# Performance work log

Measured on AMD Instinct MI355X. Metric: run time of the kernel, lower is better.

## Reference

```python
import jax, jax.numpy as jnp
import numpy as np

V, E, H, S, B, MAX_OOV = 50000, 256, 512, 500, 64, 50


def setup_inputs() -> dict:
    key = jax.random.key(0)
    ks = jax.random.split(key, 22)
    s = 0.02  # param init scale
    return {
        "input_token": jax.random.randint(ks[0], (B, 1), 0, V),
        "encoder_hidden_states": jax.random.normal(ks[1], (S, B, 2 * H), jnp.float32),
        "projected_encoder_hidden_states": jax.random.normal(ks[2], (S, B, H), jnp.float32),
        "src_mask": jnp.ones((B, S), dtype=bool),
        "prev_hidden": jax.random.normal(ks[3], (1, B, H), jnp.float32),
        "encoder_batch_extended_vocab": jax.random.randint(ks[4], (B, S), 0, V + MAX_OOV),
        "batch_max_oov": MAX_OOV,
        # learned parameters
        "emb": jax.random.normal(ks[5], (V, E), jnp.float32) * s,
        "attn_Wq": jax.random.normal(ks[6], (H, H), jnp.float32) * s,   # query_layer, no bias
        "attn_We": jax.random.normal(ks[7], (1, H), jnp.float32) * s,   # energy_layer, no bias
        "gru_Wih": jax.random.normal(ks[8], (3 * H, E + 2 * H), jnp.float32) * s,
        "gru_Whh": jax.random.normal(ks[9], (3 * H, H), jnp.float32) * s,
        "gru_bih": jax.random.normal(ks[10], (3 * H,), jnp.float32) * s,
        "gru_bhh": jax.random.normal(ks[11], (3 * H,), jnp.float32) * s,
        "lin_W": jax.random.normal(ks[12], (H, E + 3 * H), jnp.float32) * s,
        "lin_b": jax.random.normal(ks[13], (H,), jnp.float32) * s,
        "pg_W": jax.random.normal(ks[14], (1, E + 3 * H), jnp.float32) * s,
        "pg_b": jax.random.normal(ks[15], (1,), jnp.float32) * s,
        "out_W": jax.random.normal(ks[16], (V, H), jnp.float32) * s,
        "out_b": jax.random.normal(ks[17], (V,), jnp.float32) * s,
    }


def _forward(input_token, enc_h, proj_key, prev_hidden, ext_vocab, max_oov,
             emb, attn_Wq, attn_We, gru_Wih, gru_Whh, gru_bih, gru_bhh,
             lin_W, lin_b, pg_W, pg_b, out_W, out_b):
    b = input_token.shape[0]
    embed = jnp.transpose(emb[input_token], (1, 0, 2))  # [1,B,E]

    # Bahdanau attention (softmax over source dim 0; mask unused, as in source)
    q = jnp.einsum('tbh,oh->tbo', prev_hidden, attn_Wq)            # [1,B,H]
    scores = jnp.einsum('sbh,oh->sb', jnp.tanh(q + proj_key), attn_We)  # [S,B]
    alphas = jax.nn.softmax(scores, axis=0)                        # [S,B]
    context = jnp.einsum('sb,sbd->bd', alphas, enc_h)[None]        # [1,B,2H]
    attention_dist = alphas.T                                      # [B,S]

    # GRU cell (torch gate order: r, z, n)
    x = jnp.concatenate([embed, context], axis=2)[0]               # [B,E+2H]
    h = prev_hidden[0]                                             # [B,H]
    gi = x @ gru_Wih.T + gru_bih                                   # [B,3H]
    gh = h @ gru_Whh.T + gru_bhh
    i_r, i_z, i_n = jnp.split(gi, 3, axis=1)
    h_r, h_z, h_n = jnp.split(gh, 3, axis=1)
    r = jax.nn.sigmoid(i_r + h_r)
    z = jax.nn.sigmoid(i_z + h_z)
    n = jnp.tanh(i_n + r * h_n)
    h_new = (1.0 - z) * n + z * h                                  # [B,H]
    rnn_output = h_new[None]                                       # [1,B,H]

    concat = jnp.concatenate([embed, rnn_output, context], axis=2)  # [1,B,E+3H]
    p_gen = jax.nn.sigmoid(jnp.einsum('tbf,of->tbo', concat, pg_W) + pg_b)  # [1,B,1]
    lin = jnp.einsum('tbf,of->tbo', concat, lin_W) + lin_b          # [1,B,H]
    logits = jnp.einsum('tbh,vh->tbv', lin, out_W) + out_b          # [1,B,V]

    gen_prob = p_gen * jax.nn.softmax(logits, axis=2)               # [1,B,V]
    attn_prob = ((1.0 - p_gen) * attention_dist[None])[0]           # [B,S]

    ext = jnp.concatenate(
        [gen_prob, jnp.zeros((1, b, max_oov), gen_prob.dtype)], axis=2) + 1e-12  # [1,B,V+oov]
    rows = jnp.arange(b)[:, None]
    merged = ext.at[0, rows, ext_vocab].add(attn_prob)              # scatter_add over vocab dim
    output = jnp.log(merged)
    return output, h_new[None]


def reference(input_token, encoder_hidden_states, projected_encoder_hidden_states,
              src_mask, prev_hidden, encoder_batch_extended_vocab, batch_max_oov,
              emb, attn_Wq, attn_We, gru_Wih, gru_Whh, gru_bih, gru_bhh,
              lin_W, lin_b, pg_W, pg_b, out_W, out_b):
    return _forward(input_token, encoder_hidden_states, projected_encoder_hidden_states,
                    prev_hidden, encoder_batch_extended_vocab, batch_max_oov,
                    emb, attn_Wq, attn_We, gru_Wih, gru_Whh, gru_bih, gru_bhh,
                    lin_W, lin_b, pg_W, pg_b, out_W, out_b)
```

## Files before the change

### kernel.cpp

```cpp
#include <hip/hip_runtime.h>
#include <hip/hip_bf16.h>
#include <math.h>

namespace {
constexpr int V = 50000, E = 256, H = 512, S = 500, B = 64, OOVN = 50;
constexpr int VEXT = V + OOVN;
constexpr int CCAT = E + 3 * H;
constexpr int G3 = 3 * H;
constexpr int NLB = 391;

typedef __attribute__((ext_vector_type(8))) short short8;
typedef __attribute__((ext_vector_type(4))) float f32x4;

__device__ __forceinline__ float wsum(float v) {
#pragma unroll
  for (int off = 32; off > 0; off >>= 1) v += __shfl_xor(v, off, 64);
  return v;
}
__device__ __forceinline__ float sigmoidf(float x) { return 1.f / (1.f + __expf(-x)); }
__device__ __forceinline__ float fast_tanh(float x) {
  x = fminf(fmaxf(x, -15.f), 15.f);
  float e = __expf(2.f * x);
  return __fdividef(e - 1.f, e + 1.f);
}
__device__ __forceinline__ void smerge_s(float& m, float& l, float om, float ol) {
  float nm = fmaxf(m, om);
  if (nm == -INFINITY) { m = nm; return; }
  l = l * __expf(m - nm) + ol * __expf(om - nm);
  m = nm;
}

__device__ __forceinline__ short bf16_rn_s(float f) {
  __hip_bfloat16 h = __float2bfloat16(f);
  return __builtin_bit_cast(short, h);
}
__device__ __forceinline__ void hilo1(float f, short* hi, short* lo) {
  unsigned u = __float_as_uint(f);
  *hi = (short)(u >> 16);
  *lo = bf16_rn_s(f - __uint_as_float(u & 0xffff0000u));
}
__device__ __forceinline__ void hilo8(float4 a, float4 b, short8& hi, short8& lo) {
  float f[8] = {a.x, a.y, a.z, a.w, b.x, b.y, b.z, b.w};
#pragma unroll
  for (int i = 0; i < 8; ++i) {
    unsigned u = __float_as_uint(f[i]);
    hi[i] = (short)(u >> 16);
    lo[i] = bf16_rn_s(f[i] - __uint_as_float(u & 0xffff0000u));
  }
}

template <int KSTEPS>
__device__ __forceinline__ void gemm16(const short* __restrict__ Xhi,
                                       const short* __restrict__ Xlo, int ldx, int xk0,
                                       const float* __restrict__ W, int ldw, int wk0,
                                       int n0, float* __restrict__ C, int ldc) {
  const int l = threadIdx.x & 63;
  const int r16 = l & 15, q16 = l >> 4;
  f32x4 acc[4];
#pragma unroll
  for (int t = 0; t < 4; ++t) acc[t] = (f32x4){0.f, 0.f, 0.f, 0.f};

  const float* wp = W + (size_t)(n0 + r16) * ldw + wk0 + q16 * 8;
  const short* xh[4];
  const short* xl[4];
#pragma unroll
  for (int t = 0; t < 4; ++t) {
    int row = t * 16 + r16;
    xh[t] = Xhi + (size_t)row * ldx + xk0 + q16 * 8;
    xl[t] = Xlo + (size_t)row * ldx + xk0 + q16 * 8;
  }

#pragma unroll
  for (int ks = 0; ks < KSTEPS; ++ks) {
    const int ko = ks * 32;
    float4 w0 = *reinterpret_cast<const float4*>(wp + ko);
    float4 w1 = *reinterpret_cast<const float4*>(wp + ko + 4);
    short8 whi, wlo;
    hilo8(w0, w1, whi, wlo);
#pragma unroll
    for (int t = 0; t < 4; ++t) {
      short8 ah = *reinterpret_cast<const short8*>(xh[t] + ko);
      short8 al = *reinterpret_cast<const short8*>(xl[t] + ko);
      acc[t] = __builtin_amdgcn_mfma_f32_16x16x32_bf16(ah, whi, acc[t], 0, 0, 0);
      acc[t] = __builtin_amdgcn_mfma_f32_16x16x32_bf16(al, whi, acc[t], 0, 0, 0);
      acc[t] = __builtin_amdgcn_mfma_f32_16x16x32_bf16(ah, wlo, acc[t], 0, 0, 0);
    }
  }
#pragma unroll
  for (int t = 0; t < 4; ++t) {
#pragma unroll
    for (int r = 0; r < 4; ++r) {
      int row = t * 16 + q16 * 4 + r;
      C[(size_t)row * ldc + n0 + r16] = acc[t][r];
    }
  }
}

__global__ void k_prep(const int* __restrict__ tok, const float* __restrict__ emb,
                       const float* __restrict__ prevh, float* __restrict__ cc,
                       short* __restrict__ cch, short* __restrict__ ccl,
                       short* __restrict__ hh, short* __restrict__ hl) {
  int i = blockIdx.x * 256 + threadIdx.x;
  hilo1(prevh[i], &hh[i], &hl[i]);
  if (i < 16384) {
    int b = i >> 8, e = i & 255;
    float v = emb[(size_t)tok[b] * E + e];
    cc[b * CCAT + e] = v;
    hilo1(v, &cch[b * CCAT + e], &ccl[b * CCAT + e]);
  }
}

__global__ void __launch_bounds__(256) k_gemm_qgh(
    const short* __restrict__ hh, const short* __restrict__ hl,
    const float* __restrict__ Wq, const float* __restrict__ Whh,
    float* __restrict__ qpart, float* __restrict__ ghp) {
  int w = blockIdx.x * 4 + (threadIdx.x >> 6);
  if (w < 128) {
    int c = w >> 5, nt = w & 31;
    gemm16<4>(hh, hl, H, c * 128, Wq, H, c * 128, nt * 16,
              qpart + (size_t)c * 64 * H, H);
  } else {
    int w2 = w - 128;
    int c = w2 / 96, nt = w2 % 96;
    gemm16<8>(hh, hl, H, c * 256, Whh, H, c * 256, nt * 16,
              ghp + (size_t)c * 64 * G3, G3);
  }
}

__global__ void k_scores(const float* __restrict__ qpart, const float* __restrict__ pk,
                         const float* __restrict__ We, float* __restrict__ scores) {
  int lane = threadIdx.x & 63;
  int gw = blockIdx.x * 4 + (threadIdx.x >> 6);
  int s = gw >> 6, b = gw & 63;
  const float* q0 = qpart + b * H + lane * 8;
  const float* kr = pk + ((size_t)s * B + b) * H + lane * 8;
  const float* er = We + lane * 8;
  float part = 0.f;
#pragma unroll
  for (int i = 0; i < 2; ++i) {
    float4 qa = *reinterpret_cast<const float4*>(q0 + i * 4);
    float4 qb = *reinterpret_cast<const float4*>(q0 + 64 * H + i * 4);
    float4 qc = *reinterpret_cast<const float4*>(q0 + 128 * H + i * 4);
    float4 qd = *reinterpret_cast<const float4*>(q0 + 192 * H + i * 4);
    float4 kv = *reinterpret_cast<const float4*>(kr + i * 4);
    float4 ev = *reinterpret_cast<const float4*>(er + i * 4);
    part += fast_tanh(qa.x + qb.x + qc.x + qd.x + kv.x) * ev.x +
            fast_tanh(qa.y + qb.y + qc.y + qd.y + kv.y) * ev.y +
            fast_tanh(qa.z + qb.z + qc.z + qd.z + kv.z) * ev.z +
            fast_tanh(qa.w + qb.w + qc.w + qd.w + kv.w) * ev.w;
  }
  part = wsum(part);
  if (lane == 0) scores[s * B + b] = part;
}

__global__ void k_softmax_s(const float* __restrict__ scores, float* __restrict__ alphasT) {
  int b = blockIdx.x, t = threadIdx.x;
  int w = t >> 6, lane = t & 63;
  __shared__ float rm[8], rl[8];
  float v = (t < S) ? scores[t * B + b] : -INFINITY;
  float m = v;
#pragma unroll
  for (int off = 32; off > 0; off >>= 1) m = fmaxf(m, __shfl_xor(m, off, 64));
  if (lane == 0) rm[w] = m;
  __syncthreads();
  float bm = rm[0];
#pragma unroll
  for (int i = 1; i < 8; ++i) bm = fmaxf(bm, rm[i]);
  float e = (t < S) ? __expf(v - bm) : 0.f;
  float sw = wsum(e);
  if (lane == 0) rl[w] = sw;
  __syncthreads();
  float tot = rl[0];
#pragma unroll
  for (int i = 1; i < 8; ++i) tot += rl[i];
  if (t < S) alphasT[b * S + t] = e / tot;
}

__global__ void k_ctx(const float* __restrict__ alphasT, const float* __restrict__ ench,
                      float* __restrict__ ctxp) {
  int b = blockIdx.x, chf = blockIdx.y, sh = blockIdx.z;
  int t = threadIdx.x;
  __shared__ float sa[250];
  if (t < 250) sa[t] = alphasT[b * S + sh * 250 + t];
  __syncthreads();
  const float* base = ench + ((size_t)(sh * 250) * B + b) * 1024 + chf * 512 + t;
  float a0 = 0.f, a1 = 0.f;
#pragma unroll 8
  for (int s = 0; s < 250; s += 2) {
    a0 += sa[s] * base[(size_t)s * (B * 1024)];
    a1 += sa[s + 1] * base[(size_t)(s + 1) * (B * 1024)];
  }
  ctxp[((sh * B + b) * 1024) + chf * 512 + t] = a0 + a1;
}

__global__ void k_ctx2(const float* __restrict__ ctxp, float* __restrict__ cc,
                       short* __restrict__ cch, short* __restrict__ ccl) {
  int b = blockIdx.x, t = threadIdx.x;
  int c = t * 4;
  float4 v0 = *reinterpret_cast<const float4*>(&ctxp[(b * 1024) + c]);
  float4 v1 = *reinterpret_cast<const float4*>(&ctxp[((B + b) * 1024) + c]);
  float r[4] = {v0.x + v1.x, v0.y + v1.y, v0.z + v1.z, v0.w + v1.w};
#pragma unroll
  for (int i = 0; i < 4; ++i) {
    int col = 768 + c + i;
    cc[b * CCAT + col] = r[i];
    hilo1(r[i], &cch[b * CCAT + col], &ccl[b * CCAT + col]);
  }
}

__global__ void __launch_bounds__(256) k_gemm_big(
    const short* __restrict__ cch, const short* __restrict__ ccl,
    const float* __restrict__ Wih, const float* __restrict__ linW,
    float* __restrict__ gip, float* __restrict__ linpart) {
  int w = blockIdx.x * 4 + (threadIdx.x >> 6);
  if (w < 480) {
    int c = w / 96, nt = w % 96;
    int xk0 = (c == 0) ? 0 : 768 + (c - 1) * 256;
    int wk0 = c * 256;
    gemm16<8>(cch, ccl, CCAT, xk0, Wih, 1280, wk0, nt * 16,
              gip + (size_t)c * 64 * G3, G3);
  } else {
    int w2 = w - 480;
    int c = w2 >> 5, nt = w2 & 31;
    int k0 = (c == 0) ? 0 : 768 + (c - 1) * 256;
    gemm16<8>(cch, ccl, CCAT, k0, linW, CCAT, k0, nt * 16,
              linpart + (size_t)c * 64 * H, H);
  }
}

__global__ void k_gates(const float* __restrict__ gip, const float* __restrict__ ghp,
                        const float* __restrict__ bih, const float* __restrict__ bhh,
                        const float* __restrict__ prevh, const float* __restrict__ pgW,
                        const float* __restrict__ pgb, float* __restrict__ cc,
                        short* __restrict__ cch, short* __restrict__ ccl,
                        float* __restrict__ hout, float* __restrict__ pgsum) {
  int b = blockIdx.x, j = threadIdx.x;
  float ir = bih[j], iz = bih[512 + j], in_ = bih[1024 + j];
#pragma unroll
  for (int c = 0; c < 5; ++c) {
    const float* g = gip + (size_t)c * 64 * G3 + b * G3;
    ir += g[j]; iz += g[512 + j]; in_ += g[1024 + j];
  }
  float hr = bhh[j], hz = bhh[512 + j], hn = bhh[1024 + j];
#pragma unroll
  for (int c = 0; c < 2; ++c) {
    const float* g = ghp + (size_t)c * 64 * G3 + b * G3;
    hr += g[j]; hz += g[512 + j]; hn += g[1024 + j];
  }
  float r = sigmoidf(ir + hr);
  float z = sigmoidf(iz + hz);
  float n = fast_tanh(in_ + r * hn);
  float h = prevh[b * H + j];
  float hnew = (1.f - z) * n + z * h;
  hout[b * H + j] = hnew;
  cc[b * CCAT + E + j] = hnew;
  hilo1(hnew, &cch[b * CCAT + E + j], &ccl[b * CCAT + E + j]);
  float acc = hnew * pgW[E + j];
  acc += cc[b * CCAT + 768 + j] * pgW[768 + j];
  acc += cc[b * CCAT + 1280 + j] * pgW[1280 + j];
  if (j < 256) acc += cc[b * CCAT + j] * pgW[j];
  acc = wsum(acc);
  __shared__ float sl[8];
  int w = j >> 6, lane = j & 63;
  if (lane == 0) sl[w] = acc;
  __syncthreads();
  if (j == 0) {
    float tot = pgb[0];
#pragma unroll
    for (int i = 0; i < 8; ++i) tot += sl[i];
    pgsum[b] = tot;
  }
}

__global__ void __launch_bounds__(256) k_gemm_linh(const short* __restrict__ cch,
                                                   const short* __restrict__ ccl,
                                                   const float* __restrict__ linW,
                                                   float* __restrict__ linpart) {
  int w = blockIdx.x * 4 + (threadIdx.x >> 6);
  int c = w >> 5, nt = w & 31;
  int k0 = 256 + c * 256;
  gemm16<8>(cch, ccl, CCAT, k0, linW, CCAT, k0, nt * 16,
            linpart + (size_t)(5 + c) * 64 * H, H);
}

__global__ void k_linfin(const float* __restrict__ linpart, const float* __restrict__ linb,
                         short* __restrict__ lh) {
  int idx = blockIdx.x * 256 + threadIdx.x;
  int b = idx >> 9, o = idx & 511;
  float v = linb[o];
#pragma unroll
  for (int c = 0; c < 7; ++c) v += linpart[(size_t)c * 64 * H + b * H + o];
  lh[idx] = bf16_rn_s(v);
}

__global__ void __launch_bounds__(512) k_gemm_logits(
    const short* __restrict__ lh, const float* __restrict__ outW,
    const float* __restrict__ outb, float* __restrict__ logits,
    float* __restrict__ pm, float* __restrict__ pl) {
  __shared__ __align__(16) short xs[64 * 512];
  __shared__ float pml[8][64][2];
  char* xb = reinterpret_cast<char*>(xs);
  int tid = threadIdx.x;
#pragma unroll
  for (int k = 0; k < 8; ++k) {
    int m = k * 512 + tid;
    int row = m >> 6;
    short8 v = *reinterpret_cast<const short8*>(lh + (size_t)m * 8);
    int byte = (m * 16) ^ ((row & 7) << 4);
    *reinterpret_cast<short8*>(xb + byte) = v;
  }
  __syncthreads();
  const int l = tid & 63;
  const int r16 = l & 15, q16 = l >> 4;
  const int wid = tid >> 6;
  const int waveId = blockIdx.x * 8 + wid;
  const bool active = waveId < V / 16;
  if (active) {
    const int n0 = waveId * 16;
    f32x4 acc[4];
#pragma unroll
    for (int t = 0; t < 4; ++t) acc[t] = (f32x4){0.f, 0.f, 0.f, 0.f};
    const float* wp = outW + (size_t)(n0 + r16) * H + q16 * 8;
    int arow[4], aswz[4];
#pragma unroll
    for (int t = 0; t < 4; ++t) {
      int row = t * 16 + r16;
      arow[t] = row * 1024 + q16 * 16;
      aswz[t] = (row & 7) << 4;
    }
#pragma unroll
    for (int ks = 0; ks < 16; ++ks) {
      float4 w0 = *reinterpret_cast<const float4*>(wp + ks * 32);
      float4 w1 = *reinterpret_cast<const float4*>(wp + ks * 32 + 4);
      short8 wh;
      wh[0] = bf16_rn_s(w0.x); wh[1] = bf16_rn_s(w0.y);
      wh[2] = bf16_rn_s(w0.z); wh[3] = bf16_rn_s(w0.w);
      wh[4] = bf16_rn_s(w1.x); wh[5] = bf16_rn_s(w1.y);
      wh[6] = bf16_rn_s(w1.z); wh[7] = bf16_rn_s(w1.w);
#pragma unroll
      for (int t = 0; t < 4; ++t) {
        short8 a = *reinterpret_cast<const short8*>(xb + ((arow[t] + ks * 64) ^ aswz[t]));
        acc[t] = __builtin_amdgcn_mfma_f32_16x16x32_bf16(a, wh, acc[t], 0, 0, 0);
      }
    }
    float bv = outb[n0 + r16];
#pragma unroll
    for (int t = 0; t < 4; ++t) {
#pragma unroll
      for (int r = 0; r < 4; ++r) {
        float y = acc[t][r] + bv;
        int row = t * 16 + q16 * 4 + r;
        logits[(size_t)row * V + n0 + r16] = y;
        float m = y;
#pragma unroll
        for (int off = 8; off > 0; off >>= 1) m = fmaxf(m, __shfl_xor(m, off, 64));
        float e = __expf(y - m);
#pragma unroll
        for (int off = 8; off > 0; off >>= 1) e += __shfl_xor(e, off, 64);
        if (r16 == 0) { pml[wid][row][0] = m; pml[wid][row][1] = e; }
      }
    }
  } else if (r16 == 0) {
#pragma unroll
    for (int t = 0; t < 4; ++t)
#pragma unroll
      for (int r = 0; r < 4; ++r) {
        int row = t * 16 + q16 * 4 + r;
        pml[wid][row][0] = -INFINITY;
        pml[wid][row][1] = 0.f;
      }
  }
  __syncthreads();
  if (tid < 64) {
    float m = pml[0][tid][0], lv = pml[0][tid][1];
#pragma unroll
    for (int i = 1; i < 8; ++i) smerge_s(m, lv, pml[i][tid][0], pml[i][tid][1]);
    pm[blockIdx.x * 64 + tid] = m;
    pl[blockIdx.x * 64 + tid] = lv;
  }
}

__global__ void k_final(const float* __restrict__ logits, const float* __restrict__ pm,
                        const float* __restrict__ pl, const float* __restrict__ pgsum,
                        const int* __restrict__ extv, const float* __restrict__ alphasT,
                        float* __restrict__ out) {
  int b = blockIdx.x, c = blockIdx.y, t = threadIdx.x;
  __shared__ float sp_[5056];
  __shared__ float rm[4], rl[4];
  float m = -INFINITY, lv = 0.f;
  for (int i = t; i < NLB; i += 256) smerge_s(m, lv, pm[i * 64 + b], pl[i * 64 + b]);
#pragma unroll
  for (int off = 32; off > 0; off >>= 1) {
    float om = __shfl_xor(m, off, 64), ol = __shfl_xor(lv, off, 64);
    smerge_s(m, lv, om, ol);
  }
  int w = t >> 6, lane = t & 63;
  if (lane == 0) { rm[w] = m; rl[w] = lv; }
  __syncthreads();
  m = rm[0]; lv = rl[0];
#pragma unroll
  for (int i = 1; i < 4; ++i) smerge_s(m, lv, rm[i], rl[i]);
  float pg = sigmoidf(pgsum[b]);
  float scale = pg / lv;
  const int base = c * 5000;
  const int len = (c == 9) ? 5050 : 5000;
  const float* lr = logits + (size_t)b * V + base;
  for (int i = t; i < len; i += 256)
    sp_[i] = (i < 5000) ? scale * __expf(lr[i] - m) + 1e-12f : 1e-12f;
  __syncthreads();
  float wgt = 1.f - pg;
  for (int s = t; s < S; s += 256) {
    int idx = extv[b * S + s] - base;
    if ((unsigned)idx < (unsigned)len) atomicAdd(&sp_[idx], wgt * alphasT[b * S + s]);
  }
  __syncthreads();
  float* orow = out + (size_t)b * VEXT + base;
  for (int i = t; i < len; i += 256) orow[i] = logf(sp_[i]);
}
}

extern "C" void kernel_launch(void* const* d_in, const int* in_sizes, int n_in,
                              void* d_out, int out_size, void* d_ws, size_t ws_size,
                              hipStream_t stream) {
  const int*   tok   = (const int*)d_in[0];
  const float* ench  = (const float*)d_in[1];
  const float* pk    = (const float*)d_in[2];
  const float* prevh = (const float*)d_in[4];
  const int*   extv  = (const int*)d_in[5];
  const float* emb   = (const float*)d_in[7];
  const float* Wq    = (const float*)d_in[8];
  const float* We    = (const float*)d_in[9];
  const float* Wih   = (const float*)d_in[10];
  const float* Whh   = (const float*)d_in[11];
  const float* bih   = (const float*)d_in[12];
  const float* bhh   = (const float*)d_in[13];
  const float* linW  = (const float*)d_in[14];
  const float* linb  = (const float*)d_in[15];
  const float* pgW   = (const float*)d_in[16];
  const float* pgb   = (const float*)d_in[17];
  const float* outW  = (const float*)d_in[18];
  const float* outb  = (const float*)d_in[19];

  float* out = (float*)d_out;
  float* ws = (float*)d_ws;

  float* qpart   = ws;
  float* scores  = qpart + 131072;
  float* alphasT = scores + 32000;
  float* ctxp    = alphasT + 32000;
  float* cc      = ctxp + 131072;
  float* gip     = cc + 114688;
  float* ghp     = gip + 491520;
  float* linpart = ghp + 196608;
  float* pgsum   = linpart + 229376;
  float* logits  = pgsum + 64;
  float* pm      = logits + 3200000;
  float* pl      = pm + 25024;
  short* sp      = (short*)(pl + 25024);
  short* cch = sp;
  short* ccl = cch + 114688;
  short* hh  = ccl + 114688;
  short* hl  = hh + 32768;
  short* lh  = hl + 32768;
  float* hout = out + (size_t)B * VEXT;

  k_prep<<<dim3(128), dim3(256), 0, stream>>>(tok, emb, prevh, cc, cch, ccl, hh, hl);
  k_gemm_qgh<<<dim3(80), dim3(256), 0, stream>>>(hh, hl, Wq, Whh, qpart, ghp);
  k_scores<<<dim3(8000), dim3(256), 0, stream>>>(qpart, pk, We, scores);
  k_softmax_s<<<dim3(B), dim3(512), 0, stream>>>(scores, alphasT);
  k_ctx<<<dim3(64, 2, 2), dim3(512), 0, stream>>>(alphasT, ench, ctxp);
  k_ctx2<<<dim3(B), dim3(256), 0, stream>>>(ctxp, cc, cch, ccl);
  k_gemm_big<<<dim3(160), dim3(256), 0, stream>>>(cch, ccl, Wih, linW, gip, linpart);
  k_gates<<<dim3(B), dim3(512), 0, stream>>>(gip, ghp, bih, bhh, prevh, pgW, pgb, cc, cch,
                                             ccl, hout, pgsum);
  k_gemm_linh<<<dim3(16), dim3(256), 0, stream>>>(cch, ccl, linW, linpart);
  k_linfin<<<dim3(128), dim3(256), 0, stream>>>(linpart, linb, lh);
  k_gemm_logits<<<dim3(NLB), dim3(512), 0, stream>>>(lh, outW, outb, logits, pm, pl);
  k_final<<<dim3(B, 10), dim3(256), 0, stream>>>(logits, pm, pl, pgsum, extv, alphasT, out);
}
```

Before: 162.8 us.

## Fuse prep and small kernels, split activations to bf16 inside GEMMs

```diff
diff --git a/kernel.cpp b/kernel.cpp
--- a/kernel.cpp
+++ b/kernel.cpp
@@ -29,15 +29,9 @@
   l = l * __expf(m - nm) + ol * __expf(om - nm);
   m = nm;
 }
-
 __device__ __forceinline__ short bf16_rn_s(float f) {
   __hip_bfloat16 h = __float2bfloat16(f);
   return __builtin_bit_cast(short, h);
-}
-__device__ __forceinline__ void hilo1(float f, short* hi, short* lo) {
-  unsigned u = __float_as_uint(f);
-  *hi = (short)(u >> 16);
-  *lo = bf16_rn_s(f - __uint_as_float(u & 0xffff0000u));
 }
 __device__ __forceinline__ void hilo8(float4 a, float4 b, short8& hi, short8& lo) {
   float f[8] = {a.x, a.y, a.z, a.w, b.x, b.y, b.z, b.w};
@@ -50,26 +44,17 @@
 }
 
 template <int KSTEPS>
-__device__ __forceinline__ void gemm16(const short* __restrict__ Xhi,
-                                       const short* __restrict__ Xlo, int ldx, int xk0,
-                                       const float* __restrict__ W, int ldw, int wk0,
-                                       int n0, float* __restrict__ C, int ldc) {
+__device__ __forceinline__ void gemm_core_f32(const float* __restrict__ X, int ldx,
+                                              int xk0, const float* __restrict__ W,
+                                              int ldw, int wk0, int n0, f32x4 acc[4]) {
   const int l = threadIdx.x & 63;
   const int r16 = l & 15, q16 = l >> 4;
-  f32x4 acc[4];
 #pragma unroll
   for (int t = 0; t < 4; ++t) acc[t] = (f32x4){0.f, 0.f, 0.f, 0.f};
-
   const float* wp = W + (size_t)(n0 + r16) * ldw + wk0 + q16 * 8;
-  const short* xh[4];
-  const short* xl[4];
-#pragma unroll
-  for (int t = 0; t < 4; ++t) {
-    int row = t * 16 + r16;
-    xh[t] = Xhi + (size_t)row * ldx + xk0 + q16 * 8;
-    xl[t] = Xlo + (size_t)row * ldx + xk0 + q16 * 8;
-  }
-
+  const float* xp[4];
+#pragma unroll
+  for (int t = 0; t < 4; ++t) xp[t] = X + (size_t)(t * 16 + r16) * ldx + xk0 + q16 * 8;
 #pragma unroll
   for (int ks = 0; ks < KSTEPS; ++ks) {
     const int ko = ks * 32;
@@ -79,56 +64,66 @@
     hilo8(w0, w1, whi, wlo);
 #pragma unroll
     for (int t = 0; t < 4; ++t) {
-      short8 ah = *reinterpret_cast<const short8*>(xh[t] + ko);
-      short8 al = *reinterpret_cast<const short8*>(xl[t] + ko);
+      float4 x0 = *reinterpret_cast<const float4*>(xp[t] + ko);
+      float4 x1 = *reinterpret_cast<const float4*>(xp[t] + ko + 4);
+      short8 ah, al;
+      hilo8(x0, x1, ah, al);
       acc[t] = __builtin_amdgcn_mfma_f32_16x16x32_bf16(ah, whi, acc[t], 0, 0, 0);
       acc[t] = __builtin_amdgcn_mfma_f32_16x16x32_bf16(al, whi, acc[t], 0, 0, 0);
       acc[t] = __builtin_amdgcn_mfma_f32_16x16x32_bf16(ah, wlo, acc[t], 0, 0, 0);
     }
   }
-#pragma unroll
-  for (int t = 0; t < 4; ++t) {
+}
+template <int KSTEPS>
+__device__ __forceinline__ void gemm_store_f32(const float* X, int ldx, int xk0,
+                                               const float* W, int ldw, int wk0, int n0,
+                                               float* C, int ldc) {
+  f32x4 acc[4];
+  gemm_core_f32<KSTEPS>(X, ldx, xk0, W, ldw, wk0, n0, acc);
+  const int l = threadIdx.x & 63;
+  const int r16 = l & 15, q16 = l >> 4;
+#pragma unroll
+  for (int t = 0; t < 4; ++t)
 #pragma unroll
     for (int r = 0; r < 4; ++r) {
       int row = t * 16 + q16 * 4 + r;
       C[(size_t)row * ldc + n0 + r16] = acc[t][r];
     }
-  }
-}
-
-__global__ void k_prep(const int* __restrict__ tok, const float* __restrict__ emb,
-                       const float* __restrict__ prevh, float* __restrict__ cc,
-                       short* __restrict__ cch, short* __restrict__ ccl,
-                       short* __restrict__ hh, short* __restrict__ hl) {
-  int i = blockIdx.x * 256 + threadIdx.x;
-  hilo1(prevh[i], &hh[i], &hl[i]);
-  if (i < 16384) {
-    int b = i >> 8, e = i & 255;
-    float v = emb[(size_t)tok[b] * E + e];
-    cc[b * CCAT + e] = v;
-    hilo1(v, &cch[b * CCAT + e], &ccl[b * CCAT + e]);
-  }
-}
-
-__global__ void __launch_bounds__(256) k_gemm_qgh(
-    const short* __restrict__ hh, const short* __restrict__ hl,
-    const float* __restrict__ Wq, const float* __restrict__ Whh,
-    float* __restrict__ qpart, float* __restrict__ ghp) {
-  int w = blockIdx.x * 4 + (threadIdx.x >> 6);
-  if (w < 128) {
-    int c = w >> 5, nt = w & 31;
-    gemm16<4>(hh, hl, H, c * 128, Wq, H, c * 128, nt * 16,
-              qpart + (size_t)c * 64 * H, H);
+}
+
+__global__ void __launch_bounds__(256) k_head(const float* __restrict__ prevh,
+                                              const float* __restrict__ Wq,
+                                              const float* __restrict__ Whh,
+                                              const int* __restrict__ tok,
+                                              const float* __restrict__ emb,
+                                              float* __restrict__ qpart,
+                                              float* __restrict__ ghp,
+                                              float* __restrict__ cc) {
+  int gw = blockIdx.x * 4 + (threadIdx.x >> 6);
+  if (gw < 128) {
+    int c = gw >> 5, nt = gw & 31;
+    gemm_store_f32<4>(prevh, H, c * 128, Wq, H, c * 128, nt * 16,
+                      qpart + (size_t)c * 64 * H, H);
+  } else if (gw < 320) {
+    int w2 = gw - 128;
+    int c = w2 / 96, nt = w2 % 96;
+    gemm_store_f32<8>(prevh, H, c * 256, Whh, H, c * 256, nt * 16,
+                      ghp + (size_t)c * 64 * G3, G3);
   } else {
-    int w2 = w - 128;
-    int c = w2 / 96, nt = w2 % 96;
-    gemm16<8>(hh, hl, H, c * 256, Whh, H, c * 256, nt * 16,
-              ghp + (size_t)c * 64 * G3, G3);
+    int idx = (gw - 320) * 64 + (threadIdx.x & 63);
+    for (int i = idx; i < B * E; i += 1024) {
+      int b = i >> 8, e = i & 255;
+      cc[b * CCAT + e] = emb[(size_t)tok[b] * E + e];
+    }
+    for (int i = idx; i < B * 1024; i += 1024) {
+      int b = i >> 10, col = i & 1023;
+      cc[b * CCAT + 768 + col] = 0.f;
+    }
   }
 }
 
 __global__ void k_scores(const float* __restrict__ qpart, const float* __restrict__ pk,
-                         const float* __restrict__ We, float* __restrict__ scores) {
+                         const float* __restrict__ We, float* __restrict__ scoresT) {
   int lane = threadIdx.x & 63;
   int gw = blockIdx.x * 4 + (threadIdx.x >> 6);
   int s = gw >> 6, b = gw & 63;
@@ -150,14 +145,14 @@
             fast_tanh(qa.w + qb.w + qc.w + qd.w + kv.w) * ev.w;
   }
   part = wsum(part);
-  if (lane == 0) scores[s * B + b] = part;
-}
-
-__global__ void k_softmax_s(const float* __restrict__ scores, float* __restrict__ alphasT) {
+  if (lane == 0) scoresT[b * S + s] = part;
+}
+
+__global__ void k_softmax_s(const float* __restrict__ scoresT, float* __restrict__ alphasT) {
   int b = blockIdx.x, t = threadIdx.x;
   int w = t >> 6, lane = t & 63;
   __shared__ float rm[8], rl[8];
-  float v = (t < S) ? scores[t * B + b] : -INFINITY;
+  float v = (t < S) ? scoresT[b * S + t] : -INFINITY;
   float m = v;
 #pragma unroll
   for (int off = 32; off > 0; off >>= 1) m = fmaxf(m, __shfl_xor(m, off, 64));
@@ -177,54 +172,44 @@
 }
 
 __global__ void k_ctx(const float* __restrict__ alphasT, const float* __restrict__ ench,
-                      float* __restrict__ ctxp) {
-  int b = blockIdx.x, chf = blockIdx.y, sh = blockIdx.z;
+                      float* __restrict__ cc) {
+  int x = blockIdx.x;
+  int b = x >> 3, qd = (x >> 2) & 1 * 0 + ((x & 7) >> 1), sh = x & 1;
   int t = threadIdx.x;
   __shared__ float sa[250];
   if (t < 250) sa[t] = alphasT[b * S + sh * 250 + t];
   __syncthreads();
-  const float* base = ench + ((size_t)(sh * 250) * B + b) * 1024 + chf * 512 + t;
-  float a0 = 0.f, a1 = 0.f;
-#pragma unroll 8
-  for (int s = 0; s < 250; s += 2) {
+  const float* base = ench + ((size_t)(sh * 250) * B + b) * 1024 + qd * 256 + t;
+  float a0 = 0.f, a1 = 0.f, a2 = 0.f, a3 = 0.f;
+#pragma unroll 4
+  for (int s = 0; s < 248; s += 4) {
     a0 += sa[s] * base[(size_t)s * (B * 1024)];
     a1 += sa[s + 1] * base[(size_t)(s + 1) * (B * 1024)];
-  }
-  ctxp[((sh * B + b) * 1024) + chf * 512 + t] = a0 + a1;
-}
-
-__global__ void k_ctx2(const float* __restrict__ ctxp, float* __restrict__ cc,
-                       short* __restrict__ cch, short* __restrict__ ccl) {
-  int b = blockIdx.x, t = threadIdx.x;
-  int c = t * 4;
-  float4 v0 = *reinterpret_cast<const float4*>(&ctxp[(b * 1024) + c]);
-  float4 v1 = *reinterpret_cast<const float4*>(&ctxp[((B + b) * 1024) + c]);
-  float r[4] = {v0.x + v1.x, v0.y + v1.y, v0.z + v1.z, v0.w + v1.w};
-#pragma unroll
-  for (int i = 0; i < 4; ++i) {
-    int col = 768 + c + i;
-    cc[b * CCAT + col] = r[i];
-    hilo1(r[i], &cch[b * CCAT + col], &ccl[b * CCAT + col]);
-  }
-}
-
-__global__ void __launch_bounds__(256) k_gemm_big(
-    const short* __restrict__ cch, const short* __restrict__ ccl,
-    const float* __restrict__ Wih, const float* __restrict__ linW,
-    float* __restrict__ gip, float* __restrict__ linpart) {
+    a2 += sa[s + 2] * base[(size_t)(s + 2) * (B * 1024)];
+    a3 += sa[s + 3] * base[(size_t)(s + 3) * (B * 1024)];
+  }
+  a0 += sa[248] * base[(size_t)248 * (B * 1024)];
+  a1 += sa[249] * base[(size_t)249 * (B * 1024)];
+  atomicAdd(&cc[b * CCAT + 768 + qd * 256 + t], (a0 + a1) + (a2 + a3));
+}
+
+__global__ void __launch_bounds__(256) k_gemm_big(const float* __restrict__ cc,
+                                                  const float* __restrict__ Wih,
+                                                  const float* __restrict__ linW,
+                                                  float* __restrict__ gip,
+                                                  float* __restrict__ linpart) {
   int w = blockIdx.x * 4 + (threadIdx.x >> 6);
   if (w < 480) {
     int c = w / 96, nt = w % 96;
     int xk0 = (c == 0) ? 0 : 768 + (c - 1) * 256;
-    int wk0 = c * 256;
-    gemm16<8>(cch, ccl, CCAT, xk0, Wih, 1280, wk0, nt * 16,
-              gip + (size_t)c * 64 * G3, G3);
+    gemm_store_f32<8>(cc, CCAT, xk0, Wih, 1280, c * 256, nt * 16,
+                      gip + (size_t)c * 64 * G3, G3);
   } else {
     int w2 = w - 480;
     int c = w2 >> 5, nt = w2 & 31;
     int k0 = (c == 0) ? 0 : 768 + (c - 1) * 256;
-    gemm16<8>(cch, ccl, CCAT, k0, linW, CCAT, k0, nt * 16,
-              linpart + (size_t)c * 64 * H, H);
+    gemm_store_f32<8>(cc, CCAT, k0, linW, CCAT, k0, nt * 16,
+                      linpart + (size_t)c * 64 * H, H);
   }
 }
 
@@ -232,7 +217,6 @@
                         const float* __restrict__ bih, const float* __restrict__ bhh,
                         const float* __restrict__ prevh, const float* __restrict__ pgW,
                         const float* __restrict__ pgb, float* __restrict__ cc,
-                        short* __restrict__ cch, short* __restrict__ ccl,
                         float* __restrict__ hout, float* __restrict__ pgsum) {
   int b = blockIdx.x, j = threadIdx.x;
   float ir = bih[j], iz = bih[512 + j], in_ = bih[1024 + j];
@@ -254,7 +238,6 @@
   float hnew = (1.f - z) * n + z * h;
   hout[b * H + j] = hnew;
   cc[b * CCAT + E + j] = hnew;
-  hilo1(hnew, &cch[b * CCAT + E + j], &ccl[b * CCAT + E + j]);
   float acc = hnew * pgW[E + j];
   acc += cc[b * CCAT + 768 + j] * pgW[768 + j];
   acc += cc[b * CCAT + 1280 + j] * pgW[1280 + j];
@@ -272,25 +255,28 @@
   }
 }
 
-__global__ void __launch_bounds__(256) k_gemm_linh(const short* __restrict__ cch,
-                                                   const short* __restrict__ ccl,
-                                                   const float* __restrict__ linW,
-                                                   float* __restrict__ linpart) {
+__global__ void __launch_bounds__(256) k_linfin(const float* __restrict__ cc,
+                                                const float* __restrict__ linW,
+                                                const float* __restrict__ linpart,
+                                                const float* __restrict__ linb,
+                                                short* __restrict__ lh) {
   int w = blockIdx.x * 4 + (threadIdx.x >> 6);
-  int c = w >> 5, nt = w & 31;
-  int k0 = 256 + c * 256;
-  gemm16<8>(cch, ccl, CCAT, k0, linW, CCAT, k0, nt * 16,
-            linpart + (size_t)(5 + c) * 64 * H, H);
-}
-
-__global__ void k_linfin(const float* __restrict__ linpart, const float* __restrict__ linb,
-                         short* __restrict__ lh) {
-  int idx = blockIdx.x * 256 + threadIdx.x;
-  int b = idx >> 9, o = idx & 511;
-  float v = linb[o];
-#pragma unroll
-  for (int c = 0; c < 7; ++c) v += linpart[(size_t)c * 64 * H + b * H + o];
-  lh[idx] = bf16_rn_s(v);
+  f32x4 acc[4];
+  gemm_core_f32<16>(cc, CCAT, 256, linW, CCAT, 256, w * 16, acc);
+  const int l = threadIdx.x & 63;
+  const int r16 = l & 15, q16 = l >> 4;
+  int col = w * 16 + r16;
+  float bv = linb[col];
+#pragma unroll
+  for (int t = 0; t < 4; ++t)
+#pragma unroll
+    for (int r = 0; r < 4; ++r) {
+      int row = t * 16 + q16 * 4 + r;
+      float v = acc[t][r] + bv;
+#pragma unroll
+      for (int c = 0; c < 5; ++c) v += linpart[(size_t)c * 64 * H + row * H + col];
+      lh[row * H + col] = bf16_rn_s(v);
+    }
 }
 
 __global__ void __launch_bounds__(512) k_gemm_logits(
@@ -345,7 +331,7 @@
     }
     float bv = outb[n0 + r16];
 #pragma unroll
-    for (int t = 0; t < 4; ++t) {
+    for (int t = 0; t < 4; ++t)
 #pragma unroll
       for (int r = 0; r < 4; ++r) {
         float y = acc[t][r] + bv;
@@ -359,7 +345,6 @@
         for (int off = 8; off > 0; off >>= 1) e += __shfl_xor(e, off, 64);
         if (r16 == 0) { pml[wid][row][0] = m; pml[wid][row][1] = e; }
       }
-    }
   } else if (r16 == 0) {
 #pragma unroll
     for (int t = 0; t < 4; ++t)
@@ -415,7 +400,7 @@
   }
   __syncthreads();
   float* orow = out + (size_t)b * VEXT + base;
-  for (int i = t; i < len; i += 256) orow[i] = logf(sp_[i]);
+  for (int i = t; i < len; i += 256) orow[i] = __logf(sp_[i]);
 }
 }
 
@@ -445,36 +430,27 @@
   float* ws = (float*)d_ws;
 
   float* qpart   = ws;
-  float* scores  = qpart + 131072;
-  float* alphasT = scores + 32000;
-  float* ctxp    = alphasT + 32000;
-  float* cc      = ctxp + 131072;
+  float* scoresT = qpart + 131072;
+  float* alphasT = scoresT + 32000;
+  float* cc      = alphasT + 32000;
   float* gip     = cc + 114688;
   float* ghp     = gip + 491520;
   float* linpart = ghp + 196608;
-  float* pgsum   = linpart + 229376;
+  float* pgsum   = linpart + 163840;
   float* logits  = pgsum + 64;
   float* pm      = logits + 3200000;
   float* pl      = pm + 25024;
-  short* sp      = (short*)(pl + 25024);
-  short* cch = sp;
-  short* ccl = cch + 114688;
-  short* hh  = ccl + 114688;
-  short* hl  = hh + 32768;
-  short* lh  = hl + 32768;
-  float* hout = out + (size_t)B * VEXT;
-
-  k_prep<<<dim3(128), dim3(256), 0, stream>>>(tok, emb, prevh, cc, cch, ccl, hh, hl);
-  k_gemm_qgh<<<dim3(80), dim3(256), 0, stream>>>(hh, hl, Wq, Whh, qpart, ghp);
-  k_scores<<<dim3(8000), dim3(256), 0, stream>>>(qpart, pk, We, scores);
-  k_softmax_s<<<dim3(B), dim3(512), 0, stream>>>(scores, alphasT);
-  k_ctx<<<dim3(64, 2, 2), dim3(512), 0, stream>>>(alphasT, ench, ctxp);
-  k_ctx2<<<dim3(B), dim3(256), 0, stream>>>(ctxp, cc, cch, ccl);
-  k_gemm_big<<<dim3(160), dim3(256), 0, stream>>>(cch, ccl, Wih, linW, gip, linpart);
-  k_gates<<<dim3(B), dim3(512), 0, stream>>>(gip, ghp, bih, bhh, prevh, pgW, pgb, cc, cch,
-                                             ccl, hout, pgsum);
-  k_gemm_linh<<<dim3(16), dim3(256), 0, stream>>>(cch, ccl, linW, linpart);
-  k_linfin<<<dim3(128), dim3(256), 0, stream>>>(linpart, linb, lh);
+  short* lh      = (short*)(pl + 25024);
+  float* hout    = out + (size_t)B * VEXT;
+
+  k_head<<<dim3(84), dim3(256), 0, stream>>>(prevh, Wq, Whh, tok, emb, qpart, ghp, cc);
+  k_scores<<<dim3(8000), dim3(256), 0, stream>>>(qpart, pk, We, scoresT);
+  k_softmax_s<<<dim3(B), dim3(512), 0, stream>>>(scoresT, alphasT);
+  k_ctx<<<dim3(512), dim3(256), 0, stream>>>(alphasT, ench, cc);
+  k_gemm_big<<<dim3(160), dim3(256), 0, stream>>>(cc, Wih, linW, gip, linpart);
+  k_gates<<<dim3(B), dim3(512), 0, stream>>>(gip, ghp, bih, bhh, prevh, pgW, pgb, cc,
+                                             hout, pgsum);
+  k_linfin<<<dim3(8), dim3(256), 0, stream>>>(cc, linW, linpart, linb, lh);
   k_gemm_logits<<<dim3(NLB), dim3(512), 0, stream>>>(lh, outW, outb, logits, pm, pl);
   k_final<<<dim3(B, 10), dim3(256), 0, stream>>>(logits, pm, pl, pgsum, extv, alphasT, out);
 }
```

Result: faster. 149.9 us (-7.9%).
